# Kernel optimization log

Hardware: AMD Instinct MI355X
Metric: run time of the kernel (lower is better)

Reference implementation:

```python
import jax, jax.numpy as jnp
import numpy as np


def setup_inputs() -> dict:
    key = jax.random.key(0)
    k1, k2, k3 = jax.random.split(key, 3)
    in_features, out_features = 4096, 11008
    tokens = 8192
    input = jax.random.normal(k1, (tokens, in_features), dtype=jnp.float32)
    weight = jax.random.normal(k2, (out_features, in_features), dtype=jnp.float32) * 0.02
    bias = jax.random.normal(k3, (out_features,), dtype=jnp.float32) * 0.01
    return {"input": input, "weight": weight, "bias": bias}


def reference(input, weight, bias):
    # per-row absmean quantization of weight
    scale = jnp.mean(jnp.abs(weight), axis=1, keepdims=True)  # [out, 1]
    qweight = jnp.round(weight / scale) * scale               # [out, in]
    # F.linear: input @ qweight.T + bias
    return jnp.einsum('ti,oi->to', input, qweight) + bias
```

## Files before the change

### kernel.cpp

```cpp
#include <hip/hip_runtime.h>
#include <stdint.h>

#define TOKENS 8192
#define KIN    4096
#define NOUT   11008

#define BM 128
#define BN 128
#define BK 128
#define NT    (KIN / BK)
#define NTROW (TOKENS / BM)
#define NTCOL (NOUT / BN)
#define NWG   (NTROW * NTCOL)

using i32x4 = __attribute__((ext_vector_type(4))) int;

static __device__ __forceinline__ void gload_lds16(const void* g, void* l) {
  __builtin_amdgcn_global_load_lds((const __attribute__((address_space(1))) void*)g,
                                   (__attribute__((address_space(3))) void*)l,
                                   16, 0, 0);
}

static __device__ __forceinline__ int clamp_q(float f) {
  int q = (int)rintf(f);
  q = q > 127 ? 127 : q;
  q = q < -127 ? -127 : q;
  return q;
}

static __device__ __forceinline__ int pack4(int a, int b, int c, int d) {
  return (a & 0xff) | ((b & 0xff) << 8) | ((c & 0xff) << 16) | ((d & 0xff) << 24);
}

__global__ __launch_bounds__(256) void quant_fused_k(const float* __restrict__ W,
                                                     const float* __restrict__ X,
                                                     signed char* __restrict__ Wq,
                                                     signed char* __restrict__ Xq,
                                                     float* __restrict__ scale_w,
                                                     float* __restrict__ scale_x) {
  const int bid = blockIdx.x;
  const int t   = threadIdx.x;
  if (bid < NOUT) {
    const int row = bid;
    const float4* wr = reinterpret_cast<const float4*>(W + (size_t)row * KIN);
    float4 v[4];
    double s = 0.0;
#pragma unroll
    for (int i = 0; i < 4; ++i) {
      v[i] = wr[t + i * 256];
      s += fabs((double)v[i].x) + fabs((double)v[i].y) +
           fabs((double)v[i].z) + fabs((double)v[i].w);
    }
#pragma unroll
    for (int off = 32; off > 0; off >>= 1) s += __shfl_down(s, off);
    __shared__ double redd[4];
    if ((t & 63) == 0) redd[t >> 6] = s;
    __syncthreads();
    const float sc = (float)((redd[0] + redd[1] + redd[2] + redd[3]) * (1.0 / KIN));
    if (t == 0) scale_w[row] = sc;
    int* qr = reinterpret_cast<int*>(Wq + (size_t)row * KIN);
#pragma unroll
    for (int i = 0; i < 4; ++i)
      qr[t + i * 256] = pack4(clamp_q(v[i].x / sc), clamp_q(v[i].y / sc),
                              clamp_q(v[i].z / sc), clamp_q(v[i].w / sc));
  } else {
    const int row = bid - NOUT;
    const float4* xr = reinterpret_cast<const float4*>(X + (size_t)row * KIN);
    float4 v[4];
    float amax = 0.f;
#pragma unroll
    for (int i = 0; i < 4; ++i) {
      v[i] = xr[t + i * 256];
      amax = fmaxf(amax, fmaxf(fmaxf(fabsf(v[i].x), fabsf(v[i].y)),
                               fmaxf(fabsf(v[i].z), fabsf(v[i].w))));
    }
#pragma unroll
    for (int off = 32; off > 0; off >>= 1) amax = fmaxf(amax, __shfl_down(amax, off));
    __shared__ float redf[4];
    if ((t & 63) == 0) redf[t >> 6] = amax;
    __syncthreads();
    amax = fmaxf(fmaxf(redf[0], redf[1]), fmaxf(redf[2], redf[3]));
    amax = fmaxf(amax, 1e-30f);
    const float inv = 127.0f / amax;
    if (t == 0) scale_x[row] = amax * (1.0f / 127.0f);
    int* qr = reinterpret_cast<int*>(Xq + (size_t)row * KIN);
#pragma unroll
    for (int i = 0; i < 4; ++i)
      qr[t + i * 256] = pack4(clamp_q(v[i].x * inv), clamp_q(v[i].y * inv),
                              clamp_q(v[i].z * inv), clamp_q(v[i].w * inv));
  }
}

__global__ __launch_bounds__(256, 2) void gemm_k(const signed char* __restrict__ Xq,
                                                 const signed char* __restrict__ Wq,
                                                 const float* __restrict__ scale_x,
                                                 const float* __restrict__ scale_w,
                                                 const float* __restrict__ bias,
                                                 float* __restrict__ out) {
  __shared__ alignas(16) char lds[65536];

  const int xcd = (int)blockIdx.x & 7;
  const int seq = (int)blockIdx.x >> 3;
  int trow, tcol;
  if (seq < 672) {
    const int chunk = seq >> 5;
    const int rem   = seq & 31;
    trow = xcd * 8 + (rem >> 2);
    tcol = chunk * 4 + (rem & 3);
  } else {
    const int rem = seq - 672;
    trow = xcd * 8 + (rem >> 1);
    tcol = 84 + (rem & 1);
  }

  const int tid  = (int)threadIdx.x;
  const int lane = tid & 63;
  const int wave = tid >> 6;
  const int wm   = wave >> 1;
  const int wn   = wave & 1;

  const int l8 = lane >> 3;
  const size_t rowb = (size_t)KIN;
  const int swzl = ((lane & 7) ^ l8) * 16;
  const char* gA = (const char*)Xq + (size_t)(trow * BM + wave * 32 + l8) * rowb + swzl;
  const char* gB = (const char*)Wq + (size_t)(tcol * BN + wave * 32 + l8) * rowb + swzl;
  char* lA = lds + wave * 4096;
  char* lB = lds + 32768 + wave * 4096;

#define STAGE_TILE(BUF, KS) do {                                             \
    _Pragma("unroll") for (int g = 0; g < 4; ++g)                            \
      gload_lds16(gA + (size_t)(g * 8) * rowb + (KS), lA + (BUF) + g * 1024);\
    _Pragma("unroll") for (int g = 0; g < 4; ++g)                            \
      gload_lds16(gB + (size_t)(g * 8) * rowb + (KS), lB + (BUF) + g * 1024);\
  } while (0)

  const int lr = lane & 15;
  const int hi = lane >> 4;
  const int swz0 = (hi * 16) ^ ((lr & 7) << 4);
  const int swz[2] = { swz0, swz0 ^ 64 };
  const char* rdA = lds + wm * 8192 + lr * 128;
  const char* rdB = lds + 32768 + wn * 8192 + lr * 128;

  i32x4 acc[4][4];
#pragma unroll
  for (int m = 0; m < 4; ++m)
#pragma unroll
    for (int n = 0; n < 4; ++n) acc[m][n] = (i32x4){0, 0, 0, 0};
  i32x4 afr[4][2], bfr[4][2];

#define SB() __builtin_amdgcn_sched_barrier(0)

#define TILE(T, CUR) do {                                                     \
    if ((T) + 1 < NT) STAGE_TILE((CUR) ^ 16384, (size_t)((T) + 1) * 128);     \
    _Pragma("unroll") for (int mf = 0; mf < 4; ++mf) {                        \
      afr[mf][0] = *(const i32x4*)(rdA + (CUR) + mf * 2048 + swz[0]);         \
      afr[mf][1] = *(const i32x4*)(rdA + (CUR) + mf * 2048 + swz[1]);         \
    }                                                                         \
    _Pragma("unroll") for (int nf = 0; nf < 4; ++nf) {                        \
      bfr[nf][0] = *(const i32x4*)(rdB + (CUR) + nf * 2048 + swz[0]);         \
      bfr[nf][1] = *(const i32x4*)(rdB + (CUR) + nf * 2048 + swz[1]);         \
    }                                                                         \
    __builtin_amdgcn_s_setprio(1);                                            \
    _Pragma("unroll") for (int mf = 0; mf < 4; ++mf)                          \
    _Pragma("unroll") for (int nf = 0; nf < 4; ++nf)                          \
    _Pragma("unroll") for (int kk = 0; kk < 2; ++kk)                          \
      acc[mf][nf] = __builtin_amdgcn_mfma_i32_16x16x64_i8(                    \
          afr[mf][kk], bfr[nf][kk], acc[mf][nf], 0, 0, 0);                    \
    __builtin_amdgcn_s_setprio(0);                                            \
    SB();                                                                     \
    asm volatile("s_waitcnt vmcnt(0)" ::: "memory");                          \
    __builtin_amdgcn_s_barrier();                                             \
    SB();                                                                     \
  } while (0)

  STAGE_TILE(0, 0);
  asm volatile("s_waitcnt vmcnt(0)" ::: "memory");
  __builtin_amdgcn_s_barrier();
  SB();

  for (int tt = 0; tt < NT; tt += 2) {
    TILE(tt,     0);
    TILE(tt + 1, 16384);
  }

  const int gr_base = trow * BM + wm * 64 + hi * 4;
  const int gc_base = tcol * BN + wn * 64 + lr;
  float sx[4][4];
#pragma unroll
  for (int mf = 0; mf < 4; ++mf)
#pragma unroll
    for (int j = 0; j < 4; ++j) sx[mf][j] = scale_x[gr_base + mf * 16 + j];
#pragma unroll
  for (int nf = 0; nf < 4; ++nf) {
    const int gc = gc_base + nf * 16;
    const float sw = scale_w[gc];
    const float bb = bias[gc];
#pragma unroll
    for (int mf = 0; mf < 4; ++mf) {
      const size_t rb = (size_t)(gr_base + mf * 16) * NOUT + gc;
#pragma unroll
      for (int j = 0; j < 4; ++j)
        __builtin_nontemporal_store((float)acc[mf][nf][j] * (sx[mf][j] * sw) + bb,
                                    &out[rb + (size_t)j * NOUT]);
    }
  }
#undef STAGE_TILE
#undef TILE
#undef SB
}

extern "C" void kernel_launch(void* const* d_in, const int* in_sizes, int n_in,
                              void* d_out, int out_size, void* d_ws, size_t ws_size,
                              hipStream_t stream) {
  const float* X  = (const float*)d_in[0];
  const float* W  = (const float*)d_in[1];
  const float* Bi = (const float*)d_in[2];
  float* out = (float*)d_out;

  const size_t xq_bytes = (size_t)TOKENS * KIN;
  const size_t wq_bytes = (size_t)NOUT * KIN;
  const size_t need = xq_bytes + wq_bytes + (size_t)(NOUT + TOKENS) * sizeof(float);
  if (ws_size < need) return;

  char* ws = (char*)d_ws;
  signed char* Xq = (signed char*)ws;
  signed char* Wq = (signed char*)(ws + xq_bytes);
  float* scale_w = (float*)(ws + xq_bytes + wq_bytes);
  float* scale_x = scale_w + NOUT;

  quant_fused_k<<<NOUT + TOKENS, 256, 0, stream>>>(W, X, Wq, Xq, scale_w, scale_x);
  gemm_k<<<NWG, 256, 0, stream>>>(Xq, Wq, scale_x, scale_w, Bi, out);
}
```

Baseline: 434.7 us.

## Pre-pack weights in MFMA fragment order and load B directly to registers

The weight quantization kernel now writes int8 weights in a fragment-packed layout, so each lane's MFMA B operand is one contiguous 16-byte global load. The GEMM drops B staging through LDS and loads B fragments straight into double-buffered registers one tile ahead, halving LDS use. This removes LDS traffic and ds_read work for B, but B is no longer shared between the two waves with the same wn, so global/L2 traffic for B doubles and register pressure rises.

```diff
diff --git a/kernel.cpp b/kernel.cpp
--- a/kernel.cpp
+++ b/kernel.cpp
@@ -34,35 +34,43 @@
 
 __global__ __launch_bounds__(256) void quant_fused_k(const float* __restrict__ W,
                                                      const float* __restrict__ X,
-                                                     signed char* __restrict__ Wq,
+                                                     signed char* __restrict__ Bp,
                                                      signed char* __restrict__ Xq,
                                                      float* __restrict__ scale_w,
                                                      float* __restrict__ scale_x) {
   const int bid = blockIdx.x;
-  const int t   = threadIdx.x;
+  const int th  = threadIdx.x;
   if (bid < NOUT) {
-    const int row = bid;
-    const float4* wr = reinterpret_cast<const float4*>(W + (size_t)row * KIN);
+    const int c = bid;
+    const float4* wr = reinterpret_cast<const float4*>(W + (size_t)c * KIN);
     float4 v[4];
     double s = 0.0;
 #pragma unroll
     for (int i = 0; i < 4; ++i) {
-      v[i] = wr[t + i * 256];
+      v[i] = wr[th + i * 256];
       s += fabs((double)v[i].x) + fabs((double)v[i].y) +
            fabs((double)v[i].z) + fabs((double)v[i].w);
     }
 #pragma unroll
     for (int off = 32; off > 0; off >>= 1) s += __shfl_down(s, off);
     __shared__ double redd[4];
-    if ((t & 63) == 0) redd[t >> 6] = s;
+    if ((th & 63) == 0) redd[th >> 6] = s;
     __syncthreads();
     const float sc = (float)((redd[0] + redd[1] + redd[2] + redd[3]) * (1.0 / KIN));
-    if (t == 0) scale_w[row] = sc;
-    int* qr = reinterpret_cast<int*>(Wq + (size_t)row * KIN);
-#pragma unroll
-    for (int i = 0; i < 4; ++i)
-      qr[t + i * 256] = pack4(clamp_q(v[i].x / sc), clamp_q(v[i].y / sc),
-                              clamp_q(v[i].z / sc), clamp_q(v[i].w / sc));
+    if (th == 0) scale_w[c] = sc;
+    const int cb = c >> 4, ci = c & 15;
+    int* qp = reinterpret_cast<int*>(Bp + (size_t)cb * 65536);
+#pragma unroll
+    for (int i = 0; i < 4; ++i) {
+      const int w  = th + i * 256;
+      const int t  = w >> 5;
+      const int kk = (w >> 4) & 1;
+      const int hi = (w >> 2) & 3;
+      const int kb = w & 3;
+      qp[t * 512 + kk * 256 + (hi * 16 + ci) * 4 + kb] =
+          pack4(clamp_q(v[i].x / sc), clamp_q(v[i].y / sc),
+                clamp_q(v[i].z / sc), clamp_q(v[i].w / sc));
+    }
   } else {
     const int row = bid - NOUT;
     const float4* xr = reinterpret_cast<const float4*>(X + (size_t)row * KIN);
@@ -70,34 +78,34 @@
     float amax = 0.f;
 #pragma unroll
     for (int i = 0; i < 4; ++i) {
-      v[i] = xr[t + i * 256];
+      v[i] = xr[th + i * 256];
       amax = fmaxf(amax, fmaxf(fmaxf(fabsf(v[i].x), fabsf(v[i].y)),
                                fmaxf(fabsf(v[i].z), fabsf(v[i].w))));
     }
 #pragma unroll
     for (int off = 32; off > 0; off >>= 1) amax = fmaxf(amax, __shfl_down(amax, off));
     __shared__ float redf[4];
-    if ((t & 63) == 0) redf[t >> 6] = amax;
+    if ((th & 63) == 0) redf[th >> 6] = amax;
     __syncthreads();
     amax = fmaxf(fmaxf(redf[0], redf[1]), fmaxf(redf[2], redf[3]));
     amax = fmaxf(amax, 1e-30f);
     const float inv = 127.0f / amax;
-    if (t == 0) scale_x[row] = amax * (1.0f / 127.0f);
+    if (th == 0) scale_x[row] = amax * (1.0f / 127.0f);
     int* qr = reinterpret_cast<int*>(Xq + (size_t)row * KIN);
 #pragma unroll
     for (int i = 0; i < 4; ++i)
-      qr[t + i * 256] = pack4(clamp_q(v[i].x * inv), clamp_q(v[i].y * inv),
-                              clamp_q(v[i].z * inv), clamp_q(v[i].w * inv));
+      qr[th + i * 256] = pack4(clamp_q(v[i].x * inv), clamp_q(v[i].y * inv),
+                               clamp_q(v[i].z * inv), clamp_q(v[i].w * inv));
   }
 }
 
 __global__ __launch_bounds__(256, 2) void gemm_k(const signed char* __restrict__ Xq,
-                                                 const signed char* __restrict__ Wq,
+                                                 const signed char* __restrict__ Bp,
                                                  const float* __restrict__ scale_x,
                                                  const float* __restrict__ scale_w,
                                                  const float* __restrict__ bias,
                                                  float* __restrict__ out) {
-  __shared__ alignas(16) char lds[65536];
+  __shared__ alignas(16) char lds[32768];
 
   const int xcd = (int)blockIdx.x & 7;
   const int seq = (int)blockIdx.x >> 3;
@@ -123,64 +131,68 @@
   const size_t rowb = (size_t)KIN;
   const int swzl = ((lane & 7) ^ l8) * 16;
   const char* gA = (const char*)Xq + (size_t)(trow * BM + wave * 32 + l8) * rowb + swzl;
-  const char* gB = (const char*)Wq + (size_t)(tcol * BN + wave * 32 + l8) * rowb + swzl;
   char* lA = lds + wave * 4096;
-  char* lB = lds + 32768 + wave * 4096;
-
-#define STAGE_TILE(BUF, KS) do {                                             \
+
+#define STAGE_A(BUF, KS) do {                                                \
     _Pragma("unroll") for (int g = 0; g < 4; ++g)                            \
       gload_lds16(gA + (size_t)(g * 8) * rowb + (KS), lA + (BUF) + g * 1024);\
-    _Pragma("unroll") for (int g = 0; g < 4; ++g)                            \
-      gload_lds16(gB + (size_t)(g * 8) * rowb + (KS), lB + (BUF) + g * 1024);\
   } while (0)
+
+  const char* gBf = (const char*)Bp + (size_t)(tcol * 8 + wn * 4) * 65536 + lane * 16;
 
   const int lr = lane & 15;
   const int hi = lane >> 4;
   const int swz0 = (hi * 16) ^ ((lr & 7) << 4);
   const int swz[2] = { swz0, swz0 ^ 64 };
   const char* rdA = lds + wm * 8192 + lr * 128;
-  const char* rdB = lds + 32768 + wn * 8192 + lr * 128;
 
   i32x4 acc[4][4];
 #pragma unroll
   for (int m = 0; m < 4; ++m)
 #pragma unroll
     for (int n = 0; n < 4; ++n) acc[m][n] = (i32x4){0, 0, 0, 0};
-  i32x4 afr[4][2], bfr[4][2];
+  i32x4 afr[4][2];
+  i32x4 bP[4][2], bQ[4][2];
 
 #define SB() __builtin_amdgcn_sched_barrier(0)
 
-#define TILE(T, CUR) do {                                                     \
-    if ((T) + 1 < NT) STAGE_TILE((CUR) ^ 16384, (size_t)((T) + 1) * 128);     \
-    _Pragma("unroll") for (int mf = 0; mf < 4; ++mf) {                        \
-      afr[mf][0] = *(const i32x4*)(rdA + (CUR) + mf * 2048 + swz[0]);         \
-      afr[mf][1] = *(const i32x4*)(rdA + (CUR) + mf * 2048 + swz[1]);         \
-    }                                                                         \
-    _Pragma("unroll") for (int nf = 0; nf < 4; ++nf) {                        \
-      bfr[nf][0] = *(const i32x4*)(rdB + (CUR) + nf * 2048 + swz[0]);         \
-      bfr[nf][1] = *(const i32x4*)(rdB + (CUR) + nf * 2048 + swz[1]);         \
-    }                                                                         \
-    __builtin_amdgcn_s_setprio(1);                                            \
-    _Pragma("unroll") for (int mf = 0; mf < 4; ++mf)                          \
+#define LOAD_B(DST, T) do {                                                   \
     _Pragma("unroll") for (int nf = 0; nf < 4; ++nf)                          \
     _Pragma("unroll") for (int kk = 0; kk < 2; ++kk)                          \
-      acc[mf][nf] = __builtin_amdgcn_mfma_i32_16x16x64_i8(                    \
-          afr[mf][kk], bfr[nf][kk], acc[mf][nf], 0, 0, 0);                    \
-    __builtin_amdgcn_s_setprio(0);                                            \
-    SB();                                                                     \
-    asm volatile("s_waitcnt vmcnt(0)" ::: "memory");                          \
-    __builtin_amdgcn_s_barrier();                                             \
-    SB();                                                                     \
+      DST[nf][kk] = *(const i32x4*)(gBf + nf * 65536 + (T) * 2048 + kk * 1024);\
   } while (0)
 
-  STAGE_TILE(0, 0);
+#define TILE(T, CUR, BU, BNX) do {                                           \
+    if ((T) + 1 < NT) {                                                      \
+      STAGE_A((CUR) ^ 16384, (size_t)((T) + 1) * 128);                       \
+      LOAD_B(BNX, (T) + 1);                                                  \
+    }                                                                        \
+    _Pragma("unroll") for (int mf = 0; mf < 4; ++mf) {                       \
+      afr[mf][0] = *(const i32x4*)(rdA + (CUR) + mf * 2048 + swz[0]);        \
+      afr[mf][1] = *(const i32x4*)(rdA + (CUR) + mf * 2048 + swz[1]);        \
+    }                                                                        \
+    __builtin_amdgcn_s_setprio(1);                                           \
+    _Pragma("unroll") for (int mf = 0; mf < 4; ++mf)                         \
+    _Pragma("unroll") for (int nf = 0; nf < 4; ++nf)                         \
+    _Pragma("unroll") for (int kk = 0; kk < 2; ++kk)                         \
+      acc[mf][nf] = __builtin_amdgcn_mfma_i32_16x16x64_i8(                   \
+          afr[mf][kk], BU[nf][kk], acc[mf][nf], 0, 0, 0);                    \
+    __builtin_amdgcn_s_setprio(0);                                           \
+    SB();                                                                    \
+    asm volatile("s_waitcnt vmcnt(0)" ::: "memory");                         \
+    __builtin_amdgcn_s_barrier();                                            \
+    SB();                                                                    \
+  } while (0)
+
+  STAGE_A(0, 0);
+  LOAD_B(bP, 0);
   asm volatile("s_waitcnt vmcnt(0)" ::: "memory");
   __builtin_amdgcn_s_barrier();
   SB();
 
   for (int tt = 0; tt < NT; tt += 2) {
-    TILE(tt,     0);
-    TILE(tt + 1, 16384);
+    TILE(tt,     0,     bP, bQ);
+    TILE(tt + 1, 16384, bQ, bP);
   }
 
   const int gr_base = trow * BM + wm * 64 + hi * 4;
@@ -204,7 +216,8 @@
                                     &out[rb + (size_t)j * NOUT]);
     }
   }
-#undef STAGE_TILE
+#undef STAGE_A
+#undef LOAD_B
 #undef TILE
 #undef SB
 }
@@ -218,16 +231,16 @@
   float* out = (float*)d_out;
 
   const size_t xq_bytes = (size_t)TOKENS * KIN;
-  const size_t wq_bytes = (size_t)NOUT * KIN;
-  const size_t need = xq_bytes + wq_bytes + (size_t)(NOUT + TOKENS) * sizeof(float);
+  const size_t bp_bytes = (size_t)NOUT * KIN;
+  const size_t need = xq_bytes + bp_bytes + (size_t)(NOUT + TOKENS) * sizeof(float);
   if (ws_size < need) return;
 
   char* ws = (char*)d_ws;
   signed char* Xq = (signed char*)ws;
-  signed char* Wq = (signed char*)(ws + xq_bytes);
-  float* scale_w = (float*)(ws + xq_bytes + wq_bytes);
+  signed char* Bp = (signed char*)(ws + xq_bytes);
+  float* scale_w = (float*)(ws + xq_bytes + bp_bytes);
   float* scale_x = scale_w + NOUT;
 
-  quant_fused_k<<<NOUT + TOKENS, 256, 0, stream>>>(W, X, Wq, Xq, scale_w, scale_x);
-  gemm_k<<<NWG, 256, 0, stream>>>(Xq, Wq, scale_x, scale_w, Bi, out);
-}
+  quant_fused_k<<<NOUT + TOKENS, 256, 0, stream>>>(W, X, Bp, Xq, scale_w, scale_x);
+  gemm_k<<<NWG, 256, 0, stream>>>(Xq, Bp, scale_x, scale_w, Bi, out);
+}
```

Result: slower. 512.0 us (+17.8%).
